# Kernel tuning notes

Measured on AMD Instinct MI355X. Metric: run time of the kernel, lower is better.

The kernel has to match this reference:

```python
import jax, jax.numpy as jnp
import numpy as np

SCALING = 2.0  # lora alpha / rank
B, S, H = 4, 2048, 4096
N = 4096  # q/k/v out features
R = 16    # lora rank


def setup_inputs() -> dict:
    key = jax.random.key(0)
    ks = jax.random.split(key, 10)
    std_w = 1.0 / np.sqrt(H)
    inp = {
        'X': jax.random.normal(ks[0], (B, S, H), dtype=jnp.float32),
        'QW': jax.random.normal(ks[1], (N, H), dtype=jnp.float32) * std_w,
        'QA': jax.random.normal(ks[2], (R, H), dtype=jnp.float32) * std_w,
        'QB': jax.random.normal(ks[3], (N, R), dtype=jnp.float32) * 0.01,
        'KW': jax.random.normal(ks[4], (N, H), dtype=jnp.float32) * std_w,
        'KA': jax.random.normal(ks[5], (R, H), dtype=jnp.float32) * std_w,
        'KB': jax.random.normal(ks[6], (N, R), dtype=jnp.float32) * 0.01,
        'VW': jax.random.normal(ks[7], (N, H), dtype=jnp.float32) * std_w,
        'VA': jax.random.normal(ks[8], (R, H), dtype=jnp.float32) * std_w,
        'VB': jax.random.normal(ks[9], (N, R), dtype=jnp.float32) * 0.01,
    }
    return inp


def _matmul_lora(X, W, A, Bm, scaling):
    # Y = X @ W.T + scaling * (X @ A.T) @ B.T ; X: [bs, h], W: [n, h], A: [r, h], B: [n, r]
    base = jnp.einsum('bsh,nh->bsn', X, W)
    lora = jnp.einsum('bsr,nr->bsn', jnp.einsum('bsh,rh->bsr', X, A), Bm)
    return base + scaling * lora


def reference(X, QW, QA, QB, KW, KA, KB, VW, VA, VB):
    Q = _matmul_lora(X, QW, QA, QB, SCALING)
    K = _matmul_lora(X, KW, KA, KB, SCALING)
    V = _matmul_lora(X, VW, VA, VB, SCALING)
    return (Q, K, V)
```

## Files before the change

kernel.cpp:

```cpp
#include <hip/hip_runtime.h>


typedef unsigned short u16;
typedef __attribute__((ext_vector_type(4))) float  f32x4;
typedef __attribute__((ext_vector_type(8))) __bf16 bf16x8;
typedef __attribute__((ext_vector_type(8))) short  s16x8;

#define MDIM 8192
#define NDIM 4096
#define KDIM 4096

__device__ __forceinline__ u16 f2bf(float f) {
    union { float f; unsigned int u; } v;
    v.f = f;
    unsigned int r = v.u + 0x7FFFu + ((v.u >> 16) & 1u);
    return (u16)(r >> 16);
}

__global__ void __launch_bounds__(256) prep_kernel(const float* __restrict__ X,
                                                   const float* __restrict__ QW,
                                                   const float* __restrict__ QA,
                                                   const float* __restrict__ QB,
                                                   const float* __restrict__ KW,
                                                   const float* __restrict__ KA,
                                                   const float* __restrict__ KB,
                                                   const float* __restrict__ VW,
                                                   const float* __restrict__ VA,
                                                   const float* __restrict__ VB,
                                                   u16* __restrict__ Xb,
                                                   u16* __restrict__ WbAll) {
    const int bid = blockIdx.x;
    const int t   = threadIdx.x;

    if (bid >= 6144) {
        const int nvec8  = (MDIM * KDIM) / 8;
        const int stride = 2048 * 256;
        for (int i = (bid - 6144) * 256 + t; i < nvec8; i += stride) {
            f32x4 x0 = ((const f32x4*)X)[2 * i];
            f32x4 x1 = ((const f32x4*)X)[2 * i + 1];
            s16x8 o;
            o[0] = (short)f2bf(x0[0]); o[1] = (short)f2bf(x0[1]);
            o[2] = (short)f2bf(x0[2]); o[3] = (short)f2bf(x0[3]);
            o[4] = (short)f2bf(x1[0]); o[5] = (short)f2bf(x1[1]);
            o[6] = (short)f2bf(x1[2]); o[7] = (short)f2bf(x1[3]);
            ((s16x8*)Xb)[i] = o;
        }
        return;
    }

    const int z   = bid >> 11;
    const int rem = bid & 2047;
    const int hb  = (rem & 63) * 64;
    const int nb  = (rem >> 6) * 128;
    const float* W  = (z == 0) ? QW : (z == 1) ? KW : VW;
    const float* A  = (z == 0) ? QA : (z == 1) ? KA : VA;
    const float* Bm = (z == 0) ? QB : (z == 1) ? KB : VB;
    u16* Wb = WbAll + (size_t)z * NDIM * KDIM;

    __shared__ float As[16][64];
    {
        int r = t >> 4, c = (t & 15) * 4;
        *(f32x4*)&As[r][c] = *(const f32x4*)&A[r * 4096 + hb + c];
    }
    __syncthreads();

    const int hl = (t & 7) * 8;
    const int n0 = nb + (t >> 3) * 4;

    float bv[4][16];
    float s[4][8];
#pragma unroll
    for (int i = 0; i < 4; i++) {
        const float* br = &Bm[(size_t)(n0 + i) * 16];
#pragma unroll
        for (int r = 0; r < 16; r++) bv[i][r] = 2.0f * br[r];
        f32x4 w0 = *(const f32x4*)&W[(size_t)(n0 + i) * 4096 + hb + hl];
        f32x4 w1 = *(const f32x4*)&W[(size_t)(n0 + i) * 4096 + hb + hl + 4];
        s[i][0] = w0[0]; s[i][1] = w0[1]; s[i][2] = w0[2]; s[i][3] = w0[3];
        s[i][4] = w1[0]; s[i][5] = w1[1]; s[i][6] = w1[2]; s[i][7] = w1[3];
    }
#pragma unroll
    for (int r = 0; r < 16; r++) {
        f32x4 a0 = *(const f32x4*)&As[r][hl];
        f32x4 a1 = *(const f32x4*)&As[r][hl + 4];
#pragma unroll
        for (int i = 0; i < 4; i++) {
            s[i][0] += bv[i][r] * a0[0]; s[i][1] += bv[i][r] * a0[1];
            s[i][2] += bv[i][r] * a0[2]; s[i][3] += bv[i][r] * a0[3];
            s[i][4] += bv[i][r] * a1[0]; s[i][5] += bv[i][r] * a1[1];
            s[i][6] += bv[i][r] * a1[2]; s[i][7] += bv[i][r] * a1[3];
        }
    }
#pragma unroll
    for (int i = 0; i < 4; i++) {
        s16x8 o;
#pragma unroll
        for (int j = 0; j < 8; j++) o[j] = (short)f2bf(s[i][j]);
        *(s16x8*)&Wb[(size_t)(n0 + i) * 4096 + hb + hl] = o;
    }
}


#define BM 256
#define BN 256
#define BK 64

#define BAR() asm volatile("s_barrier" ::: "memory")
#define WAIT_VM(n) asm volatile("s_waitcnt vmcnt(" #n ")" ::: "memory")
#define PRIO(p) __builtin_amdgcn_s_setprio(p)

__global__ void __launch_bounds__(512, 2) gemm8_kernel(const u16* __restrict__ Xb,
                                                       const u16* __restrict__ Wb,
                                                       float* __restrict__ out) {
    extern __shared__ char lds[];

    const int t    = threadIdx.x;
    const int lane = t & 63;
    const int w    = t >> 6;
    const int wr   = w >> 2;
    const int wn   = w & 3;
    const int lr   = lane & 15;
    const int lkq  = lane >> 4;
    const int lr7  = lr & 7;

    const int orig = blockIdx.x;
    const int z    = orig >> 9;
    const int r0   = orig & 511;
    const int i_   = (r0 & 7) * 64 + (r0 >> 3);
    const int nT = i_ & 15;
    const int mT = i_ >> 4;
    const int mBase = mT * BM;
    const int nBase = nT * BN;

    const u16* Wp = Wb + (size_t)z * NDIM * KDIM;
    const char* gA = (const char*)Xb + (size_t)mBase * (KDIM * 2);
    const char* gB = (const char*)Wp + (size_t)nBase * (KDIM * 2);

    char* ldsA0 = lds;
    char* ldsA1 = lds + 32768;
    char* ldsB0 = lds + 65536;
    char* ldsB1 = lds + 98304;

    const int blkrow = lane >> 3;
    const int colswz = ((lane & 7) ^ blkrow) << 4;
    const size_t stg0 = (size_t)(((w << 1) | 0) * 8 + blkrow) * (KDIM * 2) + colswz;
    const size_t stg1 = (size_t)(((w << 1) | 1) * 8 + blkrow) * (KDIM * 2) + colswz;
    const int ldsStg0 = (((w << 1) | 0) << 10) + lane * 16;
    const int ldsStg1 = (((w << 1) | 1) << 10) + lane * 16;

#define STAGE(ldsTile, gtile, h, kt)                                              \
  { __builtin_amdgcn_global_load_lds(                                             \
        (const __attribute__((address_space(1))) void*)((gtile) + stg0 +          \
            (size_t)(h) * (128 * KDIM * 2) + (size_t)(kt) * 128),                 \
        (__attribute__((address_space(3))) void*)((ldsTile) + (h) * 16384 + ldsStg0), \
        16, 0, 0);                                                                \
    __builtin_amdgcn_global_load_lds(                                             \
        (const __attribute__((address_space(1))) void*)((gtile) + stg1 +          \
            (size_t)(h) * (128 * KDIM * 2) + (size_t)(kt) * 128),                 \
        (__attribute__((address_space(3))) void*)((ldsTile) + (h) * 16384 + ldsStg1), \
        16, 0, 0); }

    const int csA = (lkq << 4) ^ (lr7 << 4);
    const int rA0 = (wr * 128 + lr) * 128;
    const int rB0 = (wn * 64 + lr) * 128;
#define RD_A(tile, mi, kk) (*(const bf16x8*)((tile) + rA0 + (mi) * 2048 + (((kk) << 6) ^ csA)))
#define RD_B(tile, ni, kk) (*(const bf16x8*)((tile) + rB0 + (ni) * 2048 + (((kk) << 6) ^ csA)))

    f32x4 acc[8][4] = {};
    bf16x8 aR1[4][2], aR2[4][2], bR[4][2];

#define MFMA_Q(AF, mbase, nbase)                                                   \
    PRIO(1);                                                                       \
    _Pragma("unroll") for (int mi = 0; mi < 4; ++mi)                               \
    _Pragma("unroll") for (int ni = 0; ni < 2; ++ni)                               \
    _Pragma("unroll") for (int kk = 0; kk < 2; ++kk)                               \
      acc[(mbase) + mi][(nbase) + ni] = __builtin_amdgcn_mfma_f32_16x16x32_bf16(   \
          AF[mi][kk], bR[(nbase) + ni][kk], acc[(mbase) + mi][(nbase) + ni], 0, 0, 0); \
    PRIO(0);

#define PH1(pA, pB, STG)                                                           \
  { BAR();                                                                         \
    aR1[0][0] = RD_A(pA, 0, 0); aR1[0][1] = RD_A(pA, 0, 1);                        \
    bR[0][0]  = RD_B(pB, 0, 0); bR[0][1]  = RD_B(pB, 0, 1);                        \
    aR1[1][0] = RD_A(pA, 1, 0); aR1[1][1] = RD_A(pA, 1, 1);                        \
    bR[1][0]  = RD_B(pB, 1, 0); bR[1][1]  = RD_B(pB, 1, 1);                        \
    aR1[2][0] = RD_A(pA, 2, 0); aR1[2][1] = RD_A(pA, 2, 1);                        \
    aR1[3][0] = RD_A(pA, 3, 0); aR1[3][1] = RD_A(pA, 3, 1);                        \
    STG; MFMA_Q(aR1, 0, 0) }

#define PH2(pA, pB, STG)                                                           \
  { BAR();                                                                         \
    bR[2][0] = RD_B(pB, 2, 0); bR[2][1] = RD_B(pB, 2, 1);                          \
    bR[3][0] = RD_B(pB, 3, 0); bR[3][1] = RD_B(pB, 3, 1);                          \
    aR2[0][0] = RD_A(pA, 4, 0); aR2[0][1] = RD_A(pA, 4, 1);                        \
    aR2[1][0] = RD_A(pA, 5, 0); aR2[1][1] = RD_A(pA, 5, 1);                        \
    STG; MFMA_Q(aR1, 0, 2) }

#define PH3(pA, STG)                                                               \
  { BAR();                                                                         \
    aR2[2][0] = RD_A(pA, 6, 0); aR2[2][1] = RD_A(pA, 6, 1);                        \
    aR2[3][0] = RD_A(pA, 7, 0); aR2[3][1] = RD_A(pA, 7, 1);                        \
    STG; MFMA_Q(aR2, 4, 0) }

#define PH4(STG, VMW)                                                              \
  { BAR(); STG; VMW; MFMA_Q(aR2, 4, 2) }

#define PH4F()                                                                     \
  { BAR(); MFMA_Q(aR2, 4, 2) }

    STAGE(ldsA0, gA, 0, 0); STAGE(ldsA0, gA, 1, 0);
    STAGE(ldsB0, gB, 0, 0); STAGE(ldsB0, gB, 1, 0);
    STAGE(ldsB1, gB, 0, 1); STAGE(ldsB1, gB, 1, 1);
    STAGE(ldsA1, gA, 0, 1);
    WAIT_VM(6);

    for (int i = 0; i < 31; ++i) {
        const int T = 2 * i;
        PH1(ldsA0, ldsB0, STAGE(ldsA1, gA, 1, T + 1));
        PH2(ldsA0, ldsB0, );
        PH3(ldsA0,        STAGE(ldsB0, gB, 0, T + 2));
        PH4(              STAGE(ldsB0, gB, 1, T + 2), WAIT_VM(4));
        PH1(ldsA1, ldsB1, STAGE(ldsA0, gA, 0, T + 2));
        PH2(ldsA1, ldsB1, STAGE(ldsA0, gA, 1, T + 2));
        PH3(ldsA1,        STAGE(ldsB1, gB, 0, T + 3));
        PH4(              { STAGE(ldsB1, gB, 1, T + 3)
                            STAGE(ldsA1, gA, 0, T + 3) }, WAIT_VM(6));
    }

    PH1(ldsA0, ldsB0, STAGE(ldsA1, gA, 1, 63));
    PH2(ldsA0, ldsB0, );
    PH3(ldsA0, );
    PH4(, WAIT_VM(0));
    PH1(ldsA1, ldsB1, );
    PH2(ldsA1, ldsB1, );
    PH3(ldsA1, );
    PH4F();

    __syncthreads();
    float* C    = out + (size_t)z * MDIM * NDIM;
    float* ldsf = (float*)lds;
#pragma unroll
    for (int round = 0; round < 2; ++round) {
        if (wr == round) {
#pragma unroll
            for (int mi = 0; mi < 8; ++mi) {
#pragma unroll
                for (int ni = 0; ni < 4; ++ni) {
                    const int lrow = mi * 16 + lkq * 4;
                    const int col  = wn * 64 + ni * 16 + lr;
                    f32x4 v = acc[mi][ni];
#pragma unroll
                    for (int j = 0; j < 4; ++j)
                        ldsf[(lrow + j) * 256 + col] = v[j];
                }
            }
        }
        __syncthreads();
        const size_t gb = (size_t)(mBase + round * 128) * NDIM + nBase;
#pragma unroll
        for (int rr = 0; rr < 16; ++rr) {
            const int row = w * 16 + rr;
            f32x4 v = *(const f32x4*)&ldsf[row * 256 + lane * 4];
            __builtin_nontemporal_store(v,
                (f32x4*)(C + gb + (size_t)row * NDIM + lane * 4));
        }
        __syncthreads();
    }
}

extern "C" void kernel_launch(void* const* d_in, const int* in_sizes, int n_in,
                              void* d_out, int out_size, void* d_ws, size_t ws_size,
                              hipStream_t stream) {
    const float* X  = (const float*)d_in[0];
    const float* QW = (const float*)d_in[1];
    const float* QA = (const float*)d_in[2];
    const float* QB = (const float*)d_in[3];
    const float* KW = (const float*)d_in[4];
    const float* KA = (const float*)d_in[5];
    const float* KB = (const float*)d_in[6];
    const float* VW = (const float*)d_in[7];
    const float* VA = (const float*)d_in[8];
    const float* VB = (const float*)d_in[9];
    float* out = (float*)d_out;

    u16* Xb = (u16*)d_ws;
    u16* Wb = (u16*)((char*)d_ws + (size_t)MDIM * KDIM * 2);

    (void)hipFuncSetAttribute((const void*)gemm8_kernel,
                              hipFuncAttributeMaxDynamicSharedMemorySize, 131072);

    prep_kernel<<<8192, 256, 0, stream>>>(X, QW, QA, QB, KW, KA, KB,
                                          VW, VA, VB, Xb, Wb);

    gemm8_kernel<<<dim3(16 * 32 * 3), dim3(512), 131072, stream>>>(Xb, Wb, out);
}
```

Baseline: 735.6 us.

## Prefetch next tile's A/B fragments in final phase to overlap LDS reads with MFMA

Restructures the four-phase main loop so the first A fragments and all B fragments for the next K-tile are read from LDS during the last MFMA phase of the current tile, with a prologue that preloads the first tile. Global-load waits move earlier (WAIT_VM(2) in phase 3) to make sure the next buffer is ready before it is read. The aim is to hide LDS read latency behind MFMA work. The cost is more live registers and tighter ordering between the global-to-LDS staging and the fragment reads, which could cause hazards or spills.

```diff
diff --git a/kernel.cpp b/kernel.cpp
--- a/kernel.cpp
+++ b/kernel.cpp
@@ -178,32 +178,30 @@
           AF[mi][kk], bR[(nbase) + ni][kk], acc[(mbase) + mi][(nbase) + ni], 0, 0, 0); \
     PRIO(0);
 
-#define PH1(pA, pB, STG)                                                           \
-  { BAR();                                                                         \
-    aR1[0][0] = RD_A(pA, 0, 0); aR1[0][1] = RD_A(pA, 0, 1);                        \
-    bR[0][0]  = RD_B(pB, 0, 0); bR[0][1]  = RD_B(pB, 0, 1);                        \
-    aR1[1][0] = RD_A(pA, 1, 0); aR1[1][1] = RD_A(pA, 1, 1);                        \
-    bR[1][0]  = RD_B(pB, 1, 0); bR[1][1]  = RD_B(pB, 1, 1);                        \
-    aR1[2][0] = RD_A(pA, 2, 0); aR1[2][1] = RD_A(pA, 2, 1);                        \
-    aR1[3][0] = RD_A(pA, 3, 0); aR1[3][1] = RD_A(pA, 3, 1);                        \
-    STG; MFMA_Q(aR1, 0, 0) }
-
-#define PH2(pA, pB, STG)                                                           \
-  { BAR();                                                                         \
-    bR[2][0] = RD_B(pB, 2, 0); bR[2][1] = RD_B(pB, 2, 1);                          \
-    bR[3][0] = RD_B(pB, 3, 0); bR[3][1] = RD_B(pB, 3, 1);                          \
+#define PH1(pA, STG)                                                               \
+  { BAR(); STG;                                                                    \
     aR2[0][0] = RD_A(pA, 4, 0); aR2[0][1] = RD_A(pA, 4, 1);                        \
     aR2[1][0] = RD_A(pA, 5, 0); aR2[1][1] = RD_A(pA, 5, 1);                        \
-    STG; MFMA_Q(aR1, 0, 2) }
-
-#define PH3(pA, STG)                                                               \
-  { BAR();                                                                         \
+    MFMA_Q(aR1, 0, 0) }
+
+#define PH2(pA, STG)                                                               \
+  { BAR(); STG;                                                                    \
     aR2[2][0] = RD_A(pA, 6, 0); aR2[2][1] = RD_A(pA, 6, 1);                        \
     aR2[3][0] = RD_A(pA, 7, 0); aR2[3][1] = RD_A(pA, 7, 1);                        \
-    STG; MFMA_Q(aR2, 4, 0) }
-
-#define PH4(STG, VMW)                                                              \
-  { BAR(); STG; VMW; MFMA_Q(aR2, 4, 2) }
+    MFMA_Q(aR1, 0, 2) }
+
+#define PH3(STG, VMW)                                                              \
+  { BAR(); STG; VMW; MFMA_Q(aR2, 4, 0) }
+
+#define PH4(pAn, pBn, STG)                                                         \
+  { BAR(); STG;                                                                    \
+    _Pragma("unroll") for (int mi = 0; mi < 4; ++mi) {                             \
+      aR1[mi][0] = RD_A(pAn, mi, 0); aR1[mi][1] = RD_A(pAn, mi, 1); }              \
+    MFMA_Q(aR2, 4, 2)                                                              \
+    bR[0][0] = RD_B(pBn, 0, 0); bR[0][1] = RD_B(pBn, 0, 1);                        \
+    bR[1][0] = RD_B(pBn, 1, 0); bR[1][1] = RD_B(pBn, 1, 1);                        \
+    bR[2][0] = RD_B(pBn, 2, 0); bR[2][1] = RD_B(pBn, 2, 1);                        \
+    bR[3][0] = RD_B(pBn, 3, 0); bR[3][1] = RD_B(pBn, 3, 1); }
 
 #define PH4F()                                                                     \
   { BAR(); MFMA_Q(aR2, 4, 2) }
@@ -213,27 +211,36 @@
     STAGE(ldsB1, gB, 0, 1); STAGE(ldsB1, gB, 1, 1);
     STAGE(ldsA1, gA, 0, 1);
     WAIT_VM(6);
+    BAR();
+#pragma unroll
+    for (int mi = 0; mi < 4; ++mi) {
+        aR1[mi][0] = RD_A(ldsA0, mi, 0); aR1[mi][1] = RD_A(ldsA0, mi, 1);
+    }
+#pragma unroll
+    for (int ni = 0; ni < 4; ++ni) {
+        bR[ni][0] = RD_B(ldsB0, ni, 0); bR[ni][1] = RD_B(ldsB0, ni, 1);
+    }
 
     for (int i = 0; i < 31; ++i) {
         const int T = 2 * i;
-        PH1(ldsA0, ldsB0, STAGE(ldsA1, gA, 1, T + 1));
-        PH2(ldsA0, ldsB0, );
-        PH3(ldsA0,        STAGE(ldsB0, gB, 0, T + 2));
-        PH4(              STAGE(ldsB0, gB, 1, T + 2), WAIT_VM(4));
-        PH1(ldsA1, ldsB1, STAGE(ldsA0, gA, 0, T + 2));
-        PH2(ldsA1, ldsB1, STAGE(ldsA0, gA, 1, T + 2));
-        PH3(ldsA1,        STAGE(ldsB1, gB, 0, T + 3));
-        PH4(              { STAGE(ldsB1, gB, 1, T + 3)
-                            STAGE(ldsA1, gA, 0, T + 3) }, WAIT_VM(6));
-    }
-
-    PH1(ldsA0, ldsB0, STAGE(ldsA1, gA, 1, 63));
-    PH2(ldsA0, ldsB0, );
-    PH3(ldsA0, );
-    PH4(, WAIT_VM(0));
-    PH1(ldsA1, ldsB1, );
-    PH2(ldsA1, ldsB1, );
-    PH3(ldsA1, );
+        PH1(ldsA0,        STAGE(ldsA1, gA, 1, T + 1));
+        PH2(ldsA0, );
+        PH3(              STAGE(ldsB0, gB, 0, T + 2), WAIT_VM(2));
+        PH4(ldsA1, ldsB1, STAGE(ldsB0, gB, 1, T + 2));
+        PH1(ldsA1,        STAGE(ldsA0, gA, 0, T + 2));
+        PH2(ldsA1,        STAGE(ldsA0, gA, 1, T + 2));
+        PH3(              STAGE(ldsB1, gB, 0, T + 3), WAIT_VM(2));
+        PH4(ldsA0, ldsB0, { STAGE(ldsB1, gB, 1, T + 3)
+                            STAGE(ldsA1, gA, 0, T + 3) });
+    }
+
+    PH1(ldsA0,        STAGE(ldsA1, gA, 1, 63));
+    PH2(ldsA0, );
+    PH3( , WAIT_VM(0));
+    PH4(ldsA1, ldsB1, );
+    PH1(ldsA1, );
+    PH2(ldsA1, );
+    PH3( , );
     PH4F();
 
     __syncthreads();
```

Result: slower. 1.119 ms (+52.1%).
